# Performance work log

Hardware: AMD Instinct MI355X
Metric: run time of the kernel (lower is better)

## Reference

```python
import jax, jax.numpy as jnp
import numpy as np
import math

B, M, DM = 8, 512, 1024
H, DH = 16, 64
R_ATTN, R_WO, R_FF, DFF = 32, 512, 256, 4096
EPS = 1e-12  # BERT LayerNorm eps


def _layernorm(x, w, b):
    mu = jnp.mean(x, axis=-1, keepdims=True)
    var = jnp.mean(jnp.square(x - mu), axis=-1, keepdims=True)
    return (x - mu) * jax.lax.rsqrt(var + EPS) * w + b


def setup_inputs() -> dict:
    key = jax.random.key(0)
    ks = jax.random.split(key, 24)
    s = 0.02
    return {
        "x": jax.random.normal(ks[0], (B, M, DM), jnp.float32),
        "mask": jnp.zeros((B, M), jnp.float32),  # additive mask, 0 = attend
        "Pq": jax.random.normal(ks[1], (H, DM, R_ATTN), jnp.float32) * s,
        "Vq": jax.random.normal(ks[2], (H, R_ATTN, DH), jnp.float32) * s,
        "bq": jax.random.normal(ks[3], (H, DH), jnp.float32) * s,
        "Pk": jax.random.normal(ks[4], (H, DM, R_ATTN), jnp.float32) * s,
        "Vk": jax.random.normal(ks[5], (H, R_ATTN, DH), jnp.float32) * s,
        "bk": jax.random.normal(ks[6], (H, DH), jnp.float32) * s,
        "Pv": jax.random.normal(ks[7], (H, DM, R_ATTN), jnp.float32) * s,
        "Vv": jax.random.normal(ks[8], (H, R_ATTN, DH), jnp.float32) * s,
        "bv": jax.random.normal(ks[9], (H, DH), jnp.float32) * s,
        "Uo": jax.random.normal(ks[10], (DM, R_WO), jnp.float32) * s,
        "Vo": jax.random.normal(ks[11], (R_WO, DM), jnp.float32) * s,
        "bo_attn": jax.random.normal(ks[12], (DM,), jnp.float32) * s,
        "U1": jax.random.normal(ks[13], (DM, R_FF), jnp.float32) * s,
        "V1": jax.random.normal(ks[14], (R_FF, DFF), jnp.float32) * s,
        "b1": jax.random.normal(ks[15], (DFF,), jnp.float32) * s,
        "U2": jax.random.normal(ks[16], (DFF, R_FF), jnp.float32) * s,
        "V2": jax.random.normal(ks[17], (R_FF, DM), jnp.float32) * s,
        "b2": jax.random.normal(ks[18], (DM,), jnp.float32) * s,
        "ln1_w": jnp.ones((DM,), jnp.float32),
        "ln1_b": jnp.zeros((DM,), jnp.float32),
        "ln2_w": jnp.ones((DM,), jnp.float32),
        "ln2_b": jnp.zeros((DM,), jnp.float32),
    }


def reference(x, mask, Pq, Vq, bq, Pk, Vk, bk, Pv, Vv, bv,
              Uo, Vo, bo_attn, U1, V1, b1, U2, V2, b2,
              ln1_w, ln1_b, ln2_w, ln2_b):
    Bx, Mx, dm = x.shape
    dh = Vq.shape[-1]
    scale = 1.0 / math.sqrt(dh)

    def proj(P, V, b):
        # low-rank factorized per-head projection: (x @ P_h) @ V_h + b_h
        low = jnp.einsum('bmd,hdr->bhmr', x, P)      # [B,H,M,R]
        return jnp.einsum('bhmr,hrd->bhmd', low, V) + b[None, :, None, :]

    q = proj(Pq, Vq, bq)
    k = proj(Pk, Vk, bk)
    v = proj(Pv, Vv, bv)

    scores = jnp.einsum('bhmd,bhnd->bhmn', q, k) * scale
    scores = scores + mask[:, None, None, :]        # additive mask over keys
    attn = jax.nn.softmax(scores, axis=-1)
    out = jnp.einsum('bhmn,bhnd->bhmd', attn, v)    # [B,H,M,dh]
    attn_out = out.transpose(0, 2, 1, 3).reshape(Bx, Mx, dm)

    x1 = _layernorm(x + (attn_out @ Uo) @ Vo + bo_attn, ln1_w, ln1_b)

    # low-rank FFN: gelu((x1 @ U1) @ V1 + b1) @ U2 @ V2 + b2
    h = jax.nn.gelu((x1 @ U1) @ V1 + b1, approximate=False)
    y = (h @ U2) @ V2 + b2
    return _layernorm(x1 + y, ln2_w, ln2_b)
```

## Files before the change

kernel.cpp:

```cpp
#include <hip/hip_runtime.h>
#include <hip/hip_bf16.h>

typedef short short8 __attribute__((ext_vector_type(8)));
typedef float f32x4 __attribute__((ext_vector_type(4)));

#define DEV static __device__ __forceinline__

DEV unsigned short f2bu(float f) {
  __hip_bfloat16 h = __float2bfloat16(f);
  unsigned short u;
  __builtin_memcpy(&u, &h, 2);
  return u;
}
DEV float bu2f(unsigned short u) {
  union { unsigned int i; float f; } x;
  x.i = ((unsigned int)u) << 16;
  return x.f;
}

DEV float gelu_f(float v) {
  float e = __expf(-1.702f * v);
  return v * __builtin_amdgcn_rcpf(1.0f + e);
}

typedef const __attribute__((address_space(1))) unsigned int gu32;
typedef __attribute__((address_space(3))) unsigned int lu32;
DEV void gload16(const void* g, void* l) {
  __builtin_amdgcn_global_load_lds((gu32*)g, (lu32*)l, 16, 0, 0);
}

#define VMW(n) asm volatile("s_waitcnt vmcnt(" #n ")" ::: "memory")
#define LG0()  asm volatile("s_waitcnt lgkmcnt(0)" ::: "memory")
DEV void barm() {
  asm volatile("" ::: "memory");
  __builtin_amdgcn_s_barrier();
  asm volatile("" ::: "memory");
}


__global__ __launch_bounds__(256) void convx_kernel(const float* __restrict__ src,
                                                    unsigned short* __restrict__ dst, int n4) {
  int i = blockIdx.x * 256 + threadIdx.x;
  if (i >= n4) return;
  float4 v = reinterpret_cast<const float4*>(src)[i];
  ushort4 o;
  o.x = f2bu(v.x); o.y = f2bu(v.y); o.z = f2bu(v.z); o.w = f2bu(v.w);
  reinterpret_cast<ushort4*>(dst)[i] = o;
}

struct TJob {
  const float* s;
  unsigned short* d;
  long ss, ds;
  int R, C, cpt, tpb;
  int nt, pad;
};
struct TJobs { TJob j[12]; };

__global__ __launch_bounds__(256) void tconvall_kernel(TJobs js) {
  __shared__ float t[32][33];
  int idx = blockIdx.x, e = 0;
  while (idx >= js.j[e].nt) { idx -= js.j[e].nt; e++; }
  const TJob J = js.j[e];
  int bat = idx / J.tpb;
  int tt = idx - bat * J.tpb;
  int rt = tt / J.cpt, ct = tt - rt * J.cpt;
  const float* s = J.s + (size_t)bat * J.ss;
  unsigned short* d = J.d + (size_t)bat * J.ds;
  int r0 = rt * 32, c0 = ct * 32;
  int tr = threadIdx.x >> 5, tc = threadIdx.x & 31;
#pragma unroll
  for (int i = 0; i < 4; i++)
    t[tr + i * 8][tc] = s[(size_t)(r0 + tr + i * 8) * J.C + c0 + tc];
  __syncthreads();
#pragma unroll
  for (int i = 0; i < 4; i++)
    d[(size_t)(c0 + tr + i * 8) * J.R + r0 + tc] = f2bu(t[tc][tr + i * 8]);
}

#define EPI_BF16 0
#define EPI_F32  1
#define EPI_GELU 2

template <int EPI>
__global__ __launch_bounds__(256) void gemm_kernel(const unsigned short* __restrict__ A,
                                                   const unsigned short* __restrict__ Bt,
                                                   void* __restrict__ C,
                                                   const float* __restrict__ bias,
                                                   int M, int N, int K) {
  __shared__ unsigned short As0[128 * 64];
  __shared__ unsigned short Bs0[128 * 64];
  __shared__ unsigned short As1[128 * 64];
  __shared__ unsigned short Bs1[128 * 64];
  const int tid = threadIdx.x;
  const int l = tid & 63, w = tid >> 6;
  const int wm = w >> 1, wn = w & 1;
  const int lm = l & 15, lg = l >> 4;

  int nwg = gridDim.x * gridDim.y;
  int bid = blockIdx.x + gridDim.x * blockIdx.y;
  int nb = ((nwg & 7) == 0) ? ((bid & 7) * (nwg >> 3) + (bid >> 3)) : bid;
  int bm = nb % gridDim.x, bn = nb / gridDim.x;
  const int m0 = bm * 128, n0 = bn * 128;

  int klen = K, k0 = 0;
  size_t zoff = 0;
  if (gridDim.z > 1) {
    klen = K / gridDim.z;
    k0 = blockIdx.z * klen;
    zoff = (size_t)blockIdx.z * (size_t)M * (size_t)N;
  }
  float* Cf = (float*)C + zoff;
  unsigned short* Cb = (unsigned short*)C + zoff;

  f32x4 acc[4][4];
#pragma unroll
  for (int fi = 0; fi < 4; fi++)
#pragma unroll
    for (int fj = 0; fj < 4; fj++) acc[fi][fj] = (f32x4){0.f, 0.f, 0.f, 0.f};

  auto stage = [&](unsigned short* As, unsigned short* Bs, int kt) {
    const unsigned short* Ab = A + (size_t)m0 * K + k0 + kt;
    const unsigned short* Bb = Bt + (size_t)n0 * K + k0 + kt;
#pragma unroll
    for (int i = 0; i < 4; i++) {
      int c = ((w * 4 + i) << 6) + l;
      int r = c >> 3, pch = c & 7;
      int so = ((pch ^ (r & 7)) << 3);
      gload16(Ab + (size_t)r * K + so, &As[(w * 4 + i) << 9]);
      gload16(Bb + (size_t)r * K + so, &Bs[(w * 4 + i) << 9]);
    }
  };

  auto compute = [&](const unsigned short* As, const unsigned short* Bs) {
#pragma unroll
    for (int ks = 0; ks < 2; ks++) {
      short8 af[4], bfr[4];
#pragma unroll
      for (int f = 0; f < 4; f++) {
        int ra = wm * 64 + f * 16 + lm;
        af[f] = *reinterpret_cast<const short8*>(&As[(ra << 6) + (((ks * 4 + lg) ^ (ra & 7)) << 3)]);
        int rb = wn * 64 + f * 16 + lm;
        bfr[f] = *reinterpret_cast<const short8*>(&Bs[(rb << 6) + (((ks * 4 + lg) ^ (rb & 7)) << 3)]);
      }
#pragma unroll
      for (int fi = 0; fi < 4; fi++)
#pragma unroll
        for (int fj = 0; fj < 4; fj++)
          acc[fi][fj] = __builtin_amdgcn_mfma_f32_16x16x32_bf16(af[fi], bfr[fj], acc[fi][fj], 0, 0, 0);
    }
  };

  stage(As0, Bs0, 0);
  stage(As1, Bs1, 64);

  int kt = 0;
  for (; kt < klen - 128; kt += 128) {
    VMW(8); barm();
    compute(As0, Bs0);
    LG0(); barm();
    stage(As0, Bs0, kt + 128);
    VMW(8); barm();
    compute(As1, Bs1);
    LG0(); barm();
    stage(As1, Bs1, kt + 192);
  }
  VMW(8); barm();
  compute(As0, Bs0);
  VMW(0); barm();
  compute(As1, Bs1);

  float bcol[4];
  if (EPI == EPI_GELU) {
#pragma unroll
    for (int fj = 0; fj < 4; fj++) bcol[fj] = bias[n0 + wn * 64 + fj * 16 + lm];
  }

#pragma unroll
  for (int fi = 0; fi < 4; fi++) {
    int row = m0 + wm * 64 + fi * 16 + (lg << 2);
#pragma unroll
    for (int r = 0; r < 4; r++) {
      size_t rbase = (size_t)(row + r) * N;
#pragma unroll
      for (int fj = 0; fj < 4; fj++) {
        int col = n0 + wn * 64 + fj * 16 + lm;
        float v = acc[fi][fj][r];
        if (EPI == EPI_F32) {
          Cf[rbase + col] = v;
        } else if (EPI == EPI_BF16) {
          Cb[rbase + col] = f2bu(v);
        } else {
          Cb[rbase + col] = f2bu(gelu_f(v + bcol[fj]));
        }
      }
    }
  }
}

__global__ __launch_bounds__(256) void qkv_kernel(const unsigned short* __restrict__ low,
                                                  const unsigned short* __restrict__ VqT,
                                                  const unsigned short* __restrict__ VkT,
                                                  const unsigned short* __restrict__ VvT,
                                                  const float* __restrict__ bq, const float* __restrict__ bk,
                                                  const float* __restrict__ bv,
                                                  unsigned short* __restrict__ qo,
                                                  unsigned short* __restrict__ ko,
                                                  unsigned short* __restrict__ vt) {
  const int mc = blockIdx.x, h = blockIdx.y, b = blockIdx.z;
  const int tid = threadIdx.x, l = tid & 63, w = tid >> 6;
  const int lm = l & 15, lg = l >> 4;
  const int bh = b * 16 + h;
  const int m0 = mc * 128 + w * 32;

#pragma unroll
  for (int p = 0; p < 3; p++) {
    const unsigned short* VT = (p == 0 ? VqT : (p == 1 ? VkT : VvT));
    const float* bias = (p == 0 ? bq : (p == 1 ? bk : bv));
    unsigned short* out = (p == 0 ? qo : ko);
    short8 af[2];
#pragma unroll
    for (int fi = 0; fi < 2; fi++)
      af[fi] = *reinterpret_cast<const short8*>(
          low + (size_t)(b * 512 + m0 + fi * 16 + lm) * 1536 + p * 512 + h * 32 + lg * 8);
#pragma unroll
    for (int nt = 0; nt < 4; nt++) {
      short8 bf = *reinterpret_cast<const short8*>(VT + h * 2048 + (nt * 16 + lm) * 32 + lg * 8);
      float bb = bias[h * 64 + nt * 16 + lm];
#pragma unroll
      for (int fi = 0; fi < 2; fi++) {
        f32x4 acc = (f32x4){0.f, 0.f, 0.f, 0.f};
        acc = __builtin_amdgcn_mfma_f32_16x16x32_bf16(af[fi], bf, acc, 0, 0, 0);
        int row0 = m0 + fi * 16 + (lg << 2);
        if (p < 2) {
#pragma unroll
          for (int j = 0; j < 4; j++)
            out[((size_t)bh * 512 + row0 + j) * 64 + nt * 16 + lm] = f2bu(acc[j] + bb);
        } else {
          ushort4 o4;
          o4.x = f2bu(acc[0] + bb);
          o4.y = f2bu(acc[1] + bb);
          o4.z = f2bu(acc[2] + bb);
          o4.w = f2bu(acc[3] + bb);
          *reinterpret_cast<ushort4*>(
              &vt[(size_t)bh * 32768 + (size_t)(nt * 16 + lm) * 512 + row0]) = o4;
        }
      }
    }
  }
}

__global__ __launch_bounds__(256) void attn_kernel(const unsigned short* __restrict__ q,
                                                   const unsigned short* __restrict__ k,
                                                   const unsigned short* __restrict__ vt,
                                                   const float* __restrict__ mask,
                                                   unsigned short* __restrict__ attn_out) {
  __shared__ unsigned short Ks[128 * 64];
  __shared__ unsigned short Vs[64 * 128];
  __shared__ unsigned short Ps[4][32 * 128];

  int bid = blockIdx.x;
  int wid = (bid & 7) * 64 + (bid >> 3);
  const int qt = wid & 3, h = (wid >> 2) & 15, b = wid >> 6;
  const int tid = threadIdx.x, l = tid & 63, w = tid >> 6;
  const int lm = l & 15, lg = l >> 4;
  const int bh = b * 16 + h;
  const int qrow0 = qt * 128 + w * 32;

  const unsigned short* qp = q + ((size_t)bh * 512 + qrow0) * 64;
  short8 aq[2][2];
#pragma unroll
  for (int fi = 0; fi < 2; fi++)
#pragma unroll
    for (int kf = 0; kf < 2; kf++)
      aq[fi][kf] = *reinterpret_cast<const short8*>(qp + (fi * 16 + lm) * 64 + kf * 32 + (lg << 3));

  const unsigned short* kb = k + (size_t)bh * 512 * 64;
  const unsigned short* vb = vt + (size_t)bh * 64 * 512;
  const float* mk = mask + b * 512;

  short8 onesf;
#pragma unroll
  for (int j = 0; j < 8; j++) onesf[j] = (short)0x3F80;

  f32x4 oa[2][5];
#pragma unroll
  for (int fi = 0; fi < 2; fi++)
#pragma unroll
    for (int nd = 0; nd < 5; nd++) oa[fi][nd] = (f32x4){0.f, 0.f, 0.f, 0.f};

  for (int t = 0; t < 4; t++) {
    const int kbase = t * 128;
    __syncthreads();
#pragma unroll
    for (int i = 0; i < 4; i++) {
      int c = ((w * 4 + i) << 6) + l;
      int r = c >> 3, pch = c & 7;
      gload16(kb + (size_t)(kbase + r) * 64 + ((pch ^ (r & 7)) << 3), &Ks[(w * 4 + i) << 9]);
    }
#pragma unroll
    for (int i = 0; i < 4; i++) {
      int c = ((w * 4 + i) << 6) + l;
      int r = c >> 4, pch = c & 15;
      gload16(vb + (size_t)r * 512 + kbase + ((pch ^ (r & 7)) << 3), &Vs[(w * 4 + i) << 9]);
    }
    __syncthreads();

#pragma unroll
    for (int nf = 0; nf < 8; nf++) {
      int krow = nf * 16 + lm;
      int swz = krow & 7;
      short8 b0 = *reinterpret_cast<const short8*>(&Ks[(krow << 6) + ((lg ^ swz) << 3)]);
      short8 b1 = *reinterpret_cast<const short8*>(&Ks[(krow << 6) + (((4 + lg) ^ swz) << 3)]);
      float mv = mk[kbase + krow];
#pragma unroll
      for (int fi = 0; fi < 2; fi++) {
        f32x4 t0 = (f32x4){0.f, 0.f, 0.f, 0.f};
        t0 = __builtin_amdgcn_mfma_f32_16x16x32_bf16(aq[fi][0], b0, t0, 0, 0, 0);
        t0 = __builtin_amdgcn_mfma_f32_16x16x32_bf16(aq[fi][1], b1, t0, 0, 0, 0);
#pragma unroll
        for (int r = 0; r < 4; r++) {
          float e = __expf(t0[r] * 0.125f + mv);
          int prow = fi * 16 + (lg << 2) + r;
          int col = nf * 16 + lm;
          int ch = col >> 3;
          Ps[w][(prow << 7) + (((ch ^ (prow & 7)) << 3) + (col & 7))] = f2bu(e);
        }
      }
    }

#pragma unroll
    for (int kfi = 0; kfi < 4; kfi++) {
      short8 pa[2];
#pragma unroll
      for (int fi = 0; fi < 2; fi++) {
        int prow = fi * 16 + lm;
        pa[fi] = *reinterpret_cast<const short8*>(
            &Ps[w][(prow << 7) + ((((kfi << 2) + lg) ^ (prow & 7)) << 3)]);
      }
#pragma unroll
      for (int nd = 0; nd < 5; nd++) {
        short8 bv;
        if (nd < 4) {
          int vrow = nd * 16 + lm;
          bv = *reinterpret_cast<const short8*>(
              &Vs[(vrow << 7) + ((((kfi << 2) + lg) ^ (vrow & 7)) << 3)]);
        } else {
          bv = onesf;
        }
#pragma unroll
        for (int fi = 0; fi < 2; fi++)
          oa[fi][nd] = __builtin_amdgcn_mfma_f32_16x16x32_bf16(pa[fi], bv, oa[fi][nd], 0, 0, 0);
      }
    }
  }

#pragma unroll
  for (int fi = 0; fi < 2; fi++)
#pragma unroll
    for (int r = 0; r < 4; r++) {
      float inv = 1.0f / oa[fi][4][r];
      int row = qrow0 + fi * 16 + (lg << 2) + r;
#pragma unroll
      for (int nd = 0; nd < 4; nd++)
        attn_out[((size_t)b * 512 + row) * 1024 + h * 64 + nd * 16 + lm] = f2bu(oa[fi][nd][r] * inv);
    }
}

template <bool A16, bool WF, bool WB>
__global__ __launch_bounds__(256) void ln_kernel(const void* __restrict__ a,
                                                 const unsigned short* __restrict__ badd,
                                                 const float* __restrict__ bias,
                                                 const float* __restrict__ w, const float* __restrict__ bb,
                                                 float* outf, unsigned short* __restrict__ outb) {
  const int t = blockIdx.x, tid = threadIdx.x;
  float4 av;
  if (A16) {
    ushort4 u = reinterpret_cast<const ushort4*>((const unsigned short*)a + (size_t)t * 1024)[tid];
    av.x = bu2f(u.x); av.y = bu2f(u.y); av.z = bu2f(u.z); av.w = bu2f(u.w);
  } else {
    av = reinterpret_cast<const float4*>((const float*)a + (size_t)t * 1024)[tid];
  }
  ushort4 du = reinterpret_cast<const ushort4*>(badd + (size_t)t * 1024)[tid];
  float4 bi = reinterpret_cast<const float4*>(bias)[tid];
  float v0 = av.x + bu2f(du.x) + bi.x;
  float v1 = av.y + bu2f(du.y) + bi.y;
  float v2 = av.z + bu2f(du.z) + bi.z;
  float v3 = av.w + bu2f(du.w) + bi.w;
  float s = v0 + v1 + v2 + v3;
#pragma unroll
  for (int off = 32; off >= 1; off >>= 1) s += __shfl_xor(s, off);
  __shared__ float red[4], red2[4];
  if ((tid & 63) == 0) red[tid >> 6] = s;
  __syncthreads();
  float mu = (red[0] + red[1] + red[2] + red[3]) * (1.0f / 1024.0f);
  float d0 = v0 - mu, d1 = v1 - mu, d2 = v2 - mu, d3 = v3 - mu;
  float qv = d0 * d0 + d1 * d1 + d2 * d2 + d3 * d3;
#pragma unroll
  for (int off = 32; off >= 1; off >>= 1) qv += __shfl_xor(qv, off);
  if ((tid & 63) == 0) red2[tid >> 6] = qv;
  __syncthreads();
  float var = (red2[0] + red2[1] + red2[2] + red2[3]) * (1.0f / 1024.0f);
  float rs = rsqrtf(var + 1e-12f);
  float4 wv = reinterpret_cast<const float4*>(w)[tid];
  float4 bv = reinterpret_cast<const float4*>(bb)[tid];
  float4 o;
  o.x = d0 * rs * wv.x + bv.x;
  o.y = d1 * rs * wv.y + bv.y;
  o.z = d2 * rs * wv.z + bv.z;
  o.w = d3 * rs * wv.w + bv.w;
  if (WF) reinterpret_cast<float4*>(outf + (size_t)t * 1024)[tid] = o;
  if (WB) {
    ushort4 ob;
    ob.x = f2bu(o.x); ob.y = f2bu(o.y); ob.z = f2bu(o.z); ob.w = f2bu(o.w);
    reinterpret_cast<ushort4*>(outb + (size_t)t * 1024)[tid] = ob;
  }
}

template <int NP>
__global__ __launch_bounds__(256) void addcvt16_kernel(const unsigned short* __restrict__ p,
                                                       unsigned short* __restrict__ o, int n8) {
  int i = blockIdx.x * 256 + threadIdx.x;
  if (i >= n8) return;
  float s[8];
  short8 a = *reinterpret_cast<const short8*>(p + (size_t)i * 8);
#pragma unroll
  for (int e = 0; e < 8; e++) s[e] = bu2f((unsigned short)a[e]);
#pragma unroll
  for (int j = 1; j < NP; j++) {
    short8 bx = *reinterpret_cast<const short8*>(p + (size_t)j * n8 * 8 + (size_t)i * 8);
#pragma unroll
    for (int e = 0; e < 8; e++) s[e] += bu2f((unsigned short)bx[e]);
  }
  short8 ob;
#pragma unroll
  for (int e = 0; e < 8; e++) ob[e] = (short)f2bu(s[e]);
  *reinterpret_cast<short8*>(o + (size_t)i * 8) = ob;
}

extern "C" void kernel_launch(void* const* d_in, const int* in_sizes, int n_in,
                              void* d_out, int out_size, void* d_ws, size_t ws_size,
                              hipStream_t stream) {
  const float* x    = (const float*)d_in[0];
  const float* mask = (const float*)d_in[1];
  const float* Pq   = (const float*)d_in[2];
  const float* Vq   = (const float*)d_in[3];
  const float* bq   = (const float*)d_in[4];
  const float* Pk   = (const float*)d_in[5];
  const float* Vk   = (const float*)d_in[6];
  const float* bk   = (const float*)d_in[7];
  const float* Pv   = (const float*)d_in[8];
  const float* Vv   = (const float*)d_in[9];
  const float* bv   = (const float*)d_in[10];
  const float* Uo   = (const float*)d_in[11];
  const float* Vo   = (const float*)d_in[12];
  const float* bo   = (const float*)d_in[13];
  const float* U1   = (const float*)d_in[14];
  const float* V1   = (const float*)d_in[15];
  const float* b1   = (const float*)d_in[16];
  const float* U2   = (const float*)d_in[17];
  const float* V2   = (const float*)d_in[18];
  const float* b2   = (const float*)d_in[19];
  const float* ln1w = (const float*)d_in[20];
  const float* ln1b = (const float*)d_in[21];
  const float* ln2w = (const float*)d_in[22];
  const float* ln2b = (const float*)d_in[23];

  char* ws = (char*)d_ws;
  unsigned short* PcatT  = (unsigned short*)(ws + 0);
  unsigned short* UoT    = (unsigned short*)(ws + 3145728);
  unsigned short* VoT    = (unsigned short*)(ws + 4194304);
  unsigned short* U1T    = (unsigned short*)(ws + 5242880);
  unsigned short* V1T    = (unsigned short*)(ws + 5767168);
  unsigned short* U2T    = (unsigned short*)(ws + 7864320);
  unsigned short* V2T    = (unsigned short*)(ws + 9961472);
  unsigned short* xb     = (unsigned short*)(ws + 10485760);
  unsigned short* aob    = (unsigned short*)(ws + 10485760);
  unsigned short* lowb   = (unsigned short*)(ws + 18874368);
  unsigned short* t1b    = (unsigned short*)(ws + 18874368);
  unsigned short* t2b    = (unsigned short*)(ws + 20971520);
  unsigned short* qb     = (unsigned short*)(ws + 31457280);
  unsigned short* kbuf   = (unsigned short*)(ws + 39845888);
  unsigned short* vtb    = (unsigned short*)(ws + 48234496);
  unsigned short* res1b  = (unsigned short*)(ws + 31457280);
  unsigned short* skp2   = (unsigned short*)(ws + 31457280);
  unsigned short* skpo   = (unsigned short*)(ws + 56623104);
  unsigned short* yb16   = (unsigned short*)(ws + 56623104);
  unsigned short* t_ob   = (unsigned short*)(ws + 65011712);
  unsigned short* x1b    = (unsigned short*)(ws + 69206016);
  unsigned short* hb     = (unsigned short*)(ws + 77594624);
  unsigned short* skp1   = (unsigned short*)(ws + 77594624);
  unsigned short* VqT    = (unsigned short*)(ws + 110100480);
  unsigned short* VkT    = (unsigned short*)(ws + 110166016);
  unsigned short* VvT    = (unsigned short*)(ws + 110231552);
  float*          yb     = (float*)d_out;

  convx_kernel<<<4096, 256, 0, stream>>>(x, xb, 1048576);
  TJobs js;
  js.j[0]  = {Pq, PcatT + 0,       32768, 32768, 1024, 32, 1, 32, 512, 0};
  js.j[1]  = {Pk, PcatT + 524288,  32768, 32768, 1024, 32, 1, 32, 512, 0};
  js.j[2]  = {Pv, PcatT + 1048576, 32768, 32768, 1024, 32, 1, 32, 512, 0};
  js.j[3]  = {Uo, UoT, 0, 0, 1024, 512, 16, 512, 512, 0};
  js.j[4]  = {Vo, VoT, 0, 0, 512, 1024, 32, 512, 512, 0};
  js.j[5]  = {U1, U1T, 0, 0, 1024, 256, 8, 256, 256, 0};
  js.j[6]  = {V1, V1T, 0, 0, 256, 4096, 128, 1024, 1024, 0};
  js.j[7]  = {U2, U2T, 0, 0, 4096, 256, 8, 1024, 1024, 0};
  js.j[8]  = {V2, V2T, 0, 0, 256, 1024, 32, 256, 256, 0};
  js.j[9]  = {Vq, VqT, 2048, 2048, 32, 64, 2, 2, 32, 0};
  js.j[10] = {Vk, VkT, 2048, 2048, 32, 64, 2, 2, 32, 0};
  js.j[11] = {Vv, VvT, 2048, 2048, 32, 64, 2, 2, 32, 0};
  tconvall_kernel<<<5216, 256, 0, stream>>>(js);

  gemm_kernel<EPI_BF16><<<dim3(32, 12), 256, 0, stream>>>(xb, PcatT, lowb, nullptr, 4096, 1536, 1024);

  qkv_kernel<<<dim3(4, 16, 8), 256, 0, stream>>>(lowb, VqT, VkT, VvT, bq, bk, bv, qb, kbuf, vtb);

  attn_kernel<<<512, 256, 0, stream>>>(qb, kbuf, vtb, mask, aob);

  gemm_kernel<EPI_BF16><<<dim3(32, 4, 2), 256, 0, stream>>>(aob, UoT, skpo, nullptr, 4096, 512, 1024);
  addcvt16_kernel<2><<<1024, 256, 0, stream>>>(skpo, t_ob, 262144);
  gemm_kernel<EPI_BF16><<<dim3(32, 8), 256, 0, stream>>>(t_ob, VoT, res1b, nullptr, 4096, 1024, 512);

  ln_kernel<false, false, true><<<4096, 256, 0, stream>>>(x, res1b, bo, ln1w, ln1b, nullptr, x1b);

  gemm_kernel<EPI_BF16><<<dim3(32, 2, 4), 256, 0, stream>>>(x1b, U1T, skp1, nullptr, 4096, 256, 1024);
  addcvt16_kernel<4><<<512, 256, 0, stream>>>(skp1, t1b, 131072);
  gemm_kernel<EPI_GELU><<<dim3(32, 32), 256, 0, stream>>>(t1b, V1T, hb, b1, 4096, 4096, 256);
  gemm_kernel<EPI_BF16><<<dim3(32, 2, 4), 256, 0, stream>>>(hb, U2T, skp2, nullptr, 4096, 256, 4096);
  addcvt16_kernel<4><<<512, 256, 0, stream>>>(skp2, t2b, 131072);
  gemm_kernel<EPI_BF16><<<dim3(32, 8), 256, 0, stream>>>(t2b, V2T, yb16, nullptr, 4096, 1024, 256);

  ln_kernel<true, true, false><<<4096, 256, 0, stream>>>(x1b, yb16, b2, ln2w, ln2b, yb, nullptr);

  (void)in_sizes; (void)n_in; (void)out_size; (void)ws_size;
}
```

Measured before the change: 164.1 us.

## Fuse FFN up-projection, GELU and U2 projection into one kernel

Adds ffn2_kernel, which computes gelu(t1@V1+b1) per 128-wide hidden chunk into shared memory and immediately multiplies it by U2, accumulating split-K partials over 8 hidden slices. This removes the write and reread of the large 4096x4096 bf16 hidden activation and one launch. In exchange, the V1 GEMM is recomputed once per output column tile (two tiles), the split-K reduction grows to eight partials, and the second GEMM phase loads U2 without overlap.

```diff
diff --git a/kernel.cpp b/kernel.cpp
--- a/kernel.cpp
+++ b/kernel.cpp
@@ -80,13 +80,11 @@
 
 #define EPI_BF16 0
 #define EPI_F32  1
-#define EPI_GELU 2
 
 template <int EPI>
 __global__ __launch_bounds__(256) void gemm_kernel(const unsigned short* __restrict__ A,
                                                    const unsigned short* __restrict__ Bt,
                                                    void* __restrict__ C,
-                                                   const float* __restrict__ bias,
                                                    int M, int N, int K) {
   __shared__ unsigned short As0[128 * 64];
   __shared__ unsigned short Bs0[128 * 64];
@@ -170,12 +168,6 @@
   VMW(0); barm();
   compute(As1, Bs1);
 
-  float bcol[4];
-  if (EPI == EPI_GELU) {
-#pragma unroll
-    for (int fj = 0; fj < 4; fj++) bcol[fj] = bias[n0 + wn * 64 + fj * 16 + lm];
-  }
-
 #pragma unroll
   for (int fi = 0; fi < 4; fi++) {
     int row = m0 + wm * 64 + fi * 16 + (lg << 2);
@@ -186,13 +178,155 @@
       for (int fj = 0; fj < 4; fj++) {
         int col = n0 + wn * 64 + fj * 16 + lm;
         float v = acc[fi][fj][r];
-        if (EPI == EPI_F32) {
-          Cf[rbase + col] = v;
-        } else if (EPI == EPI_BF16) {
-          Cb[rbase + col] = f2bu(v);
-        } else {
-          Cb[rbase + col] = f2bu(gelu_f(v + bcol[fj]));
+        if (EPI == EPI_F32) Cf[rbase + col] = v;
+        else Cb[rbase + col] = f2bu(v);
+      }
+    }
+  }
+}
+
+__global__ __launch_bounds__(256) void ffn2_kernel(const unsigned short* __restrict__ t1,
+                                                   const unsigned short* __restrict__ V1T,
+                                                   const unsigned short* __restrict__ U2T,
+                                                   const float* __restrict__ b1,
+                                                   unsigned short* __restrict__ t2p) {
+  __shared__ char smem[65536];
+  unsigned short* As0 = (unsigned short*)smem;
+  unsigned short* Bs0 = (unsigned short*)(smem + 16384);
+  unsigned short* As1 = (unsigned short*)(smem + 32768);
+  unsigned short* Bs1 = (unsigned short*)(smem + 49152);
+  unsigned short* Ps  = (unsigned short*)smem;
+  unsigned short* U2s = (unsigned short*)(smem + 32768);
+
+  const int tid = threadIdx.x, l = tid & 63, w = tid >> 6;
+  const int wm = w >> 1, wn = w & 1;
+  const int lm = l & 15, lg = l >> 4;
+
+  const int m0 = blockIdx.x * 128;
+  const int r0 = blockIdx.y * 128;
+  const int fz = blockIdx.z;
+
+  f32x4 acc2[4][4];
+#pragma unroll
+  for (int fi = 0; fi < 4; fi++)
+#pragma unroll
+    for (int fj = 0; fj < 4; fj++) acc2[fi][fj] = (f32x4){0.f, 0.f, 0.f, 0.f};
+
+  for (int ft = 0; ft < 4; ft++) {
+    const int f0 = fz * 512 + ft * 128;
+
+    f32x4 acc1[4][4];
+#pragma unroll
+    for (int fi = 0; fi < 4; fi++)
+#pragma unroll
+      for (int fj = 0; fj < 4; fj++) acc1[fi][fj] = (f32x4){0.f, 0.f, 0.f, 0.f};
+
+    auto stage1 = [&](unsigned short* As, unsigned short* Bs, int kt) {
+      const unsigned short* Ab = t1 + (size_t)m0 * 256 + kt;
+      const unsigned short* Bb = V1T + (size_t)f0 * 256 + kt;
+#pragma unroll
+      for (int i = 0; i < 4; i++) {
+        int c = ((w * 4 + i) << 6) + l;
+        int r = c >> 3, pch = c & 7;
+        int so = ((pch ^ (r & 7)) << 3);
+        gload16(Ab + (size_t)r * 256 + so, &As[(w * 4 + i) << 9]);
+        gload16(Bb + (size_t)r * 256 + so, &Bs[(w * 4 + i) << 9]);
+      }
+    };
+    auto compute1 = [&](const unsigned short* As, const unsigned short* Bs) {
+#pragma unroll
+      for (int ks = 0; ks < 2; ks++) {
+        short8 af[4], bfr[4];
+#pragma unroll
+        for (int f = 0; f < 4; f++) {
+          int ra = wm * 64 + f * 16 + lm;
+          af[f] = *reinterpret_cast<const short8*>(&As[(ra << 6) + (((ks * 4 + lg) ^ (ra & 7)) << 3)]);
+          int rb = wn * 64 + f * 16 + lm;
+          bfr[f] = *reinterpret_cast<const short8*>(&Bs[(rb << 6) + (((ks * 4 + lg) ^ (rb & 7)) << 3)]);
         }
+#pragma unroll
+        for (int fi = 0; fi < 4; fi++)
+#pragma unroll
+          for (int fj = 0; fj < 4; fj++)
+            acc1[fi][fj] = __builtin_amdgcn_mfma_f32_16x16x32_bf16(af[fi], bfr[fj], acc1[fi][fj], 0, 0, 0);
+      }
+    };
+
+    stage1(As0, Bs0, 0);
+    stage1(As1, Bs1, 64);
+    VMW(8); barm();
+    compute1(As0, Bs0);
+    LG0(); barm();
+    stage1(As0, Bs0, 128);
+    VMW(8); barm();
+    compute1(As1, Bs1);
+    LG0(); barm();
+    stage1(As1, Bs1, 192);
+    VMW(8); barm();
+    compute1(As0, Bs0);
+    VMW(0); barm();
+    compute1(As1, Bs1);
+    barm();
+
+    float b1f[4];
+#pragma unroll
+    for (int fj = 0; fj < 4; fj++) b1f[fj] = b1[f0 + wn * 64 + fj * 16 + lm];
+#pragma unroll
+    for (int fi = 0; fi < 4; fi++)
+#pragma unroll
+      for (int fj = 0; fj < 4; fj++)
+#pragma unroll
+        for (int r = 0; r < 4; r++) {
+          int row = wm * 64 + fi * 16 + (lg << 2) + r;
+          int col = wn * 64 + fj * 16 + lm;
+          int ch = col >> 3;
+          Ps[(row << 7) + (((ch ^ (row & 15)) << 3) + (col & 7))] =
+              f2bu(gelu_f(acc1[fi][fj][r] + b1f[fj]));
+        }
+
+#pragma unroll
+    for (int i = 0; i < 8; i++) {
+      int c = i * 256 + tid;
+      int rr = c >> 4, pch = c & 15;
+      gload16(U2T + (size_t)(r0 + rr) * 4096 + f0 + ((pch ^ (rr & 15)) << 3), &U2s[c << 3]);
+    }
+    LG0(); VMW(0); barm();
+
+#pragma unroll
+    for (int ks = 0; ks < 4; ks++) {
+      short8 pa[4], ub[4];
+#pragma unroll
+      for (int fi = 0; fi < 4; fi++) {
+        int row = wm * 64 + fi * 16 + lm;
+        pa[fi] = *reinterpret_cast<const short8*>(
+            &Ps[(row << 7) + (((ks * 4 + lg) ^ (row & 15)) << 3)]);
+      }
+#pragma unroll
+      for (int fj = 0; fj < 4; fj++) {
+        int rr = wn * 64 + fj * 16 + lm;
+        ub[fj] = *reinterpret_cast<const short8*>(
+            &U2s[(rr << 7) + (((ks * 4 + lg) ^ (rr & 15)) << 3)]);
+      }
+#pragma unroll
+      for (int fi = 0; fi < 4; fi++)
+#pragma unroll
+        for (int fj = 0; fj < 4; fj++)
+          acc2[fi][fj] = __builtin_amdgcn_mfma_f32_16x16x32_bf16(pa[fi], ub[fj], acc2[fi][fj], 0, 0, 0);
+    }
+    barm();
+  }
+
+  unsigned short* out = t2p + (size_t)fz * 4096 * 256;
+#pragma unroll
+  for (int fi = 0; fi < 4; fi++) {
+    int row = m0 + wm * 64 + fi * 16 + (lg << 2);
+#pragma unroll
+    for (int r = 0; r < 4; r++) {
+      size_t rbase = (size_t)(row + r) * 256;
+#pragma unroll
+      for (int fj = 0; fj < 4; fj++) {
+        int col = r0 + wn * 64 + fj * 16 + lm;
+        out[rbase + col] = f2bu(acc2[fi][fj][r]);
       }
     }
   }
@@ -483,13 +617,12 @@
   unsigned short* kbuf   = (unsigned short*)(ws + 39845888);
   unsigned short* vtb    = (unsigned short*)(ws + 48234496);
   unsigned short* res1b  = (unsigned short*)(ws + 31457280);
-  unsigned short* skp2   = (unsigned short*)(ws + 31457280);
   unsigned short* skpo   = (unsigned short*)(ws + 56623104);
   unsigned short* yb16   = (unsigned short*)(ws + 56623104);
   unsigned short* t_ob   = (unsigned short*)(ws + 65011712);
   unsigned short* x1b    = (unsigned short*)(ws + 69206016);
-  unsigned short* hb     = (unsigned short*)(ws + 77594624);
-  unsigned short* skp1   = (unsigned short*)(ws + 77594624);
+  unsigned short* t2p    = (unsigned short*)(ws + 77594624);
+  unsigned short* skp1   = (unsigned short*)(ws + 94371840);
   unsigned short* VqT    = (unsigned short*)(ws + 110100480);
   unsigned short* VkT    = (unsigned short*)(ws + 110166016);
   unsigned short* VvT    = (unsigned short*)(ws + 110231552);
@@ -511,24 +644,23 @@
   js.j[11] = {Vv, VvT, 2048, 2048, 32, 64, 2, 2, 32, 0};
   tconvall_kernel<<<5216, 256, 0, stream>>>(js);
 
-  gemm_kernel<EPI_BF16><<<dim3(32, 12), 256, 0, stream>>>(xb, PcatT, lowb, nullptr, 4096, 1536, 1024);
+  gemm_kernel<EPI_BF16><<<dim3(32, 12), 256, 0, stream>>>(xb, PcatT, lowb, 4096, 1536, 1024);
 
   qkv_kernel<<<dim3(4, 16, 8), 256, 0, stream>>>(lowb, VqT, VkT, VvT, bq, bk, bv, qb, kbuf, vtb);
 
   attn_kernel<<<512, 256, 0, stream>>>(qb, kbuf, vtb, mask, aob);
 
-  gemm_kernel<EPI_BF16><<<dim3(32, 4, 2), 256, 0, stream>>>(aob, UoT, skpo, nullptr, 4096, 512, 1024);
+  gemm_kernel<EPI_BF16><<<dim3(32, 4, 2), 256, 0, stream>>>(aob, UoT, skpo, 4096, 512, 1024);
   addcvt16_kernel<2><<<1024, 256, 0, stream>>>(skpo, t_ob, 262144);
-  gemm_kernel<EPI_BF16><<<dim3(32, 8), 256, 0, stream>>>(t_ob, VoT, res1b, nullptr, 4096, 1024, 512);
+  gemm_kernel<EPI_BF16><<<dim3(32, 8), 256, 0, stream>>>(t_ob, VoT, res1b, 4096, 1024, 512);
 
   ln_kernel<false, false, true><<<4096, 256, 0, stream>>>(x, res1b, bo, ln1w, ln1b, nullptr, x1b);
 
-  gemm_kernel<EPI_BF16><<<dim3(32, 2, 4), 256, 0, stream>>>(x1b, U1T, skp1, nullptr, 4096, 256, 1024);
+  gemm_kernel<EPI_BF16><<<dim3(32, 2, 4), 256, 0, stream>>>(x1b, U1T, skp1, 4096, 256, 1024);
   addcvt16_kernel<4><<<512, 256, 0, stream>>>(skp1, t1b, 131072);
-  gemm_kernel<EPI_GELU><<<dim3(32, 32), 256, 0, stream>>>(t1b, V1T, hb, b1, 4096, 4096, 256);
-  gemm_kernel<EPI_BF16><<<dim3(32, 2, 4), 256, 0, stream>>>(hb, U2T, skp2, nullptr, 4096, 256, 4096);
-  addcvt16_kernel<4><<<512, 256, 0, stream>>>(skp2, t2b, 131072);
-  gemm_kernel<EPI_BF16><<<dim3(32, 8), 256, 0, stream>>>(t2b, V2T, yb16, nullptr, 4096, 1024, 256);
+  ffn2_kernel<<<dim3(32, 2, 8), 256, 0, stream>>>(t1b, V1T, U2T, b1, t2p);
+  addcvt16_kernel<8><<<512, 256, 0, stream>>>(t2p, t2b, 131072);
+  gemm_kernel<EPI_BF16><<<dim3(32, 8), 256, 0, stream>>>(t2b, V2T, yb16, 4096, 1024, 256);
 
   ln_kernel<true, true, false><<<4096, 256, 0, stream>>>(x1b, yb16, b2, ln2w, ln2b, yb, nullptr);
 
```

After: 181.4 us. 1.11x slower.
